# Performance work log

Hardware: AMD Instinct MI355X
Metric: run time of the kernel (lower is better)

Reference implementation:

```python
import jax, jax.numpy as jnp
import numpy as np

B, F, N = 8, 64, 256
EPS = 1e-09


def setup_inputs() -> dict:
    key = jax.random.key(0)
    k = jax.random.split(key, 4)
    x = jax.random.normal(k[0], (B, F, N, N), dtype=jnp.float32)
    mask = jax.random.randint(k[1], (B, N), 0, 2).astype(jnp.float32)
    weight = jnp.ones((1, F, 1, 1), dtype=jnp.float32)
    weight_exp = jax.random.normal(k[2], (1, F, 1, 1), dtype=jnp.float32)
    weight_bias = jnp.zeros((1, F, 1, 1), dtype=jnp.float32)
    bias = jax.random.normal(k[3], (1, F, 1), dtype=jnp.float32)
    return dict(x=x, mask=mask, weight=weight, weight_exp=weight_exp,
                weight_bias=weight_bias, bias=bias)


def reference(x, mask, weight, weight_exp, weight_bias, bias):
    # mask: [B, N] -> pairwise mask [B, 1, N, N] (broadcast over features,
    # same math as torch .expand to [B, F, N, N])
    m2 = mask[:, None, :, None] * mask[:, None, None, :]
    mdiag = mask * mask                       # diagonal of pairwise mask, [B, N]
    n = jnp.sum(mdiag, axis=-1, keepdims=True)  # [B, 1] (identical across F)
    n2 = jnp.clip(n - 1.0, 1.0)

    # trace(A * mask) per (b, f)
    diagA = jnp.einsum('bfii->bfi', x)
    trace = jnp.sum(diagA * mdiag[:, None, :], axis=-1)        # [B, F]
    # trace(A^2 * mask): diag(A @ A)_i = sum_k A[i,k] A[k,i]  (O(N^2), same math
    # as torch.linalg.matrix_power(A, 2) followed by masked diagonal trace)
    diagA2 = jnp.einsum('bfik,bfki->bfi', x, x)
    trace_sq = jnp.sum(diagA2 * mdiag[:, None, :], axis=-1)    # [B, F]

    mean = trace / n
    variance = trace_sq / n2 - trace ** 2 / (n * n2)
    mean_b = mean.mean(axis=1)      # [B]
    var_b = variance.mean(axis=1)   # [B]

    eye = jnp.eye(N, dtype=x.dtype)
    m_t = mean_b[:, None, None, None] * eye          # diag_embed of mean
    x_centered = (x - m_t) * m2
    x_norm = x_centered / jnp.sqrt(var_b[:, None, None, None] + EPS)

    bias_diag = bias[..., None] * eye                # [1, F, N, N] diag_embed
    return x_norm * (weight * jnp.exp(weight_exp) + weight_bias) + bias_diag
```

## Files before the change

kernel.cpp:

```cpp
#include <hip/hip_runtime.h>
#include <math.h>

#define BB 8
#define FF 64
#define NN 256
#define EPSF 1e-9f

typedef float floatx4 __attribute__((ext_vector_type(4)));


__global__ __launch_bounds__(256) void k_traces(const float* __restrict__ x,
                                                const float* __restrict__ mask,
                                                float* __restrict__ ws) {
    __shared__ float md[NN];
    __shared__ float T1[64][65];
    __shared__ float T2[64][65];
    __shared__ float red[4][2];
    const int t    = threadIdx.x;
    const int bh   = blockIdx.x;
    const int bf   = bh >> 1;
    const int half = bh & 1;
    const int b    = bf >> 6;
    const float* __restrict__ xm = x + (size_t)bf * (NN * NN);

    {
        float m = mask[b * NN + t];
        md[t] = m * m;
    }
    __syncthreads();

    const int lane = t & 63;
    const int w    = t >> 6;
    float acc2 = 0.f;
    float trp  = 0.f;

    constexpr int IT0[5] = {0, 1, 0, 0, 0};
    constexpr int KT0[5] = {0, 1, 1, 2, 3};
    constexpr int IT1[5] = {2, 3, 1, 1, 2};
    constexpr int KT1[5] = {2, 3, 2, 3, 3};

    #pragma unroll
    for (int e = 0; e < 5; ++e) {
        const int it = half ? IT1[e] : IT0[e];
        const int kt = half ? KT1[e] : KT0[e];
        const int i0 = it << 6;
        const int k0 = kt << 6;
        const bool diag = (it == kt);
        #pragma unroll
        for (int rr = 0; rr < 4; ++rr) {
            int idx4 = t + (rr << 8);
            int a    = idx4 >> 4;
            int c4   = (idx4 & 15) << 2;
            float4 v = *(const float4*)(xm + (size_t)(i0 + a) * NN + k0 + c4);
            T1[a][c4 + 0] = v.x; T1[a][c4 + 1] = v.y;
            T1[a][c4 + 2] = v.z; T1[a][c4 + 3] = v.w;
            if (!diag) {
                float4 u = *(const float4*)(xm + (size_t)(k0 + a) * NN + i0 + c4);
                T2[a][c4 + 0] = u.x; T2[a][c4 + 1] = u.y;
                T2[a][c4 + 2] = u.z; T2[a][c4 + 3] = u.w;
            }
        }
        __syncthreads();
        if (!diag) {
            #pragma unroll
            for (int s = 0; s < 16; ++s) {
                int a = w + (s << 2);
                acc2 += T1[a][lane] * T2[lane][a] * (md[i0 + a] + md[k0 + lane]);
            }
        } else {
            #pragma unroll
            for (int s = 0; s < 16; ++s) {
                int a = w + (s << 2);
                acc2 += T1[a][lane] * T1[lane][a] * md[i0 + a];
                if (lane == a) trp += T1[a][a] * md[i0 + a];
            }
        }
        __syncthreads();
    }

    #pragma unroll
    for (int off = 32; off > 0; off >>= 1) {
        acc2 += __shfl_down(acc2, off);
        trp  += __shfl_down(trp,  off);
    }
    if (lane == 0) { red[w][0] = trp; red[w][1] = acc2; }
    __syncthreads();
    if (t == 0) {
        float trace = red[0][0] + red[1][0] + red[2][0] + red[3][0];
        float tsq   = red[0][1] + red[1][1] + red[2][1] + red[3][1];
        ws[bh]        = trace;
        ws[1024 + bh] = tsq;
    }
}

__global__ __launch_bounds__(512) void k_finish(const float* __restrict__ mask,
                                                const float* __restrict__ wt,
                                                const float* __restrict__ wexp,
                                                const float* __restrict__ wbias,
                                                float* __restrict__ ws) {
    const int t    = threadIdx.x;
    const int b    = t >> 6;
    const int lane = t & 63;
    float trace = ws[2 * t] + ws[2 * t + 1];
    float tsq   = ws[1024 + 2 * t] + ws[1024 + 2 * t + 1];
    float tr2   = trace * trace;
    float nn = 0.f;
    #pragma unroll
    for (int r = 0; r < 4; ++r) {
        float m = mask[b * NN + lane + (r << 6)];
        nn += m * m;
    }
    #pragma unroll
    for (int off = 32; off > 0; off >>= 1) {
        trace += __shfl_down(trace, off);
        tr2   += __shfl_down(tr2, off);
        tsq   += __shfl_down(tsq, off);
        nn    += __shfl_down(nn, off);
    }
    if (lane == 0) {
        float n  = nn;
        float n2 = fmaxf(n - 1.f, 1.f);
        float mean_b = trace / (64.f * n);
        float var_b  = tsq / (64.f * n2) - tr2 / (64.f * n * n2);
        ws[2048 + b] = mean_b;
        ws[2056 + b] = 1.f / sqrtf(var_b + EPSF);
    }
    if (t < FF) ws[2064 + t] = wt[t] * expf(wexp[t]) + wbias[t];
}

__global__ __launch_bounds__(256) void k_out(const float* __restrict__ x,
                                             const float* __restrict__ mask,
                                             const float* __restrict__ bias,
                                             const float* __restrict__ ws,
                                             float* __restrict__ out) {
    const int total4 = (BB * FF * NN * NN) >> 2;
    const int stride = gridDim.x * blockDim.x;
    for (int idx4 = blockIdx.x * blockDim.x + threadIdx.x; idx4 < total4; idx4 += stride) {
        int e = idx4 << 2;
        int j = e & (NN - 1);
        int i = (e >> 8) & (NN - 1);
        int f = (e >> 16) & (FF - 1);
        int b = e >> 22;
        float4 xv = ((const float4*)x)[idx4];
        float  mi = mask[(b << 8) + i];
        float4 mj = ((const float4*)mask)[((b << 8) + j) >> 2];
        float meanb   = ws[2048 + b];
        float inv_std = ws[2056 + b];
        float g  = ws[2064 + f];
        float bs = bias[f];
        float s  = mi * inv_std * g;
        floatx4 o;
        o.x = (xv.x - (i == j     ? meanb : 0.f)) * mj.x * s + (i == j     ? bs : 0.f);
        o.y = (xv.y - (i == j + 1 ? meanb : 0.f)) * mj.y * s + (i == j + 1 ? bs : 0.f);
        o.z = (xv.z - (i == j + 2 ? meanb : 0.f)) * mj.z * s + (i == j + 2 ? bs : 0.f);
        o.w = (xv.w - (i == j + 3 ? meanb : 0.f)) * mj.w * s + (i == j + 3 ? bs : 0.f);
        __builtin_nontemporal_store(o, &((floatx4*)out)[idx4]);
    }
}

extern "C" void kernel_launch(void* const* d_in, const int* in_sizes, int n_in,
                              void* d_out, int out_size, void* d_ws, size_t ws_size,
                              hipStream_t stream) {
    const float* x     = (const float*)d_in[0];
    const float* mask  = (const float*)d_in[1];
    const float* wt    = (const float*)d_in[2];
    const float* wexp  = (const float*)d_in[3];
    const float* wbias = (const float*)d_in[4];
    const float* bias  = (const float*)d_in[5];
    float* out = (float*)d_out;
    float* ws  = (float*)d_ws;

    hipLaunchKernelGGL(k_traces, dim3(BB * FF * 2), dim3(256), 0, stream, x, mask, ws);
    hipLaunchKernelGGL(k_finish, dim3(1),           dim3(512), 0, stream, mask, wt, wexp, wbias, ws);
    hipLaunchKernelGGL(k_out,    dim3(2048),        dim3(256), 0, stream, x, mask, bias, ws, out);
}
```

Baseline: 66.41 us.

## Fold finish kernel into output kernel and register-prefetch trace tiles

Removes the single-block finish kernel: every block of the output kernel now recomputes per-batch mean, inverse std and the per-feature gains from the partial traces and keeps them in shared memory. This drops one launch and its serialized tail, at the cost of 2048 blocks each repeating the small reduction. The trace kernel also prefetches the next tile pair into registers while the current tile is being computed, so global loads overlap the LDS compute. Tile ordering is fixed so that the first two steps are the diagonal tiles.

```diff
diff --git a/kernel.cpp b/kernel.cpp
--- a/kernel.cpp
+++ b/kernel.cpp
@@ -8,6 +8,17 @@
 
 typedef float floatx4 __attribute__((ext_vector_type(4)));
 
+
+__device__ __forceinline__ int jit(int half, int e) {
+    constexpr int IT0[5] = {0, 1, 0, 0, 0};
+    constexpr int IT1[5] = {2, 3, 1, 1, 2};
+    return half ? IT1[e] : IT0[e];
+}
+__device__ __forceinline__ int jkt(int half, int e) {
+    constexpr int KT0[5] = {0, 1, 1, 2, 3};
+    constexpr int KT1[5] = {2, 3, 2, 3, 3};
+    return half ? KT1[e] : KT0[e];
+}
 
 __global__ __launch_bounds__(256) void k_traces(const float* __restrict__ x,
                                                 const float* __restrict__ mask,
@@ -23,44 +34,55 @@
     const int b    = bf >> 6;
     const float* __restrict__ xm = x + (size_t)bf * (NN * NN);
 
-    {
-        float m = mask[b * NN + t];
-        md[t] = m * m;
-    }
-    __syncthreads();
+    { float m = mask[b * NN + t]; md[t] = m * m; }
 
     const int lane = t & 63;
     const int w    = t >> 6;
-    float acc2 = 0.f;
-    float trp  = 0.f;
+    const int la   = t >> 4;
+    const int lc4  = (t & 15) << 2;
+    float acc2 = 0.f, trp = 0.f;
 
-    constexpr int IT0[5] = {0, 1, 0, 0, 0};
-    constexpr int KT0[5] = {0, 1, 1, 2, 3};
-    constexpr int IT1[5] = {2, 3, 1, 1, 2};
-    constexpr int KT1[5] = {2, 3, 2, 3, 3};
+    float4 p1[4], p2[4];
+
+    {
+        const int i0 = jit(half, 0) << 6, k0 = jkt(half, 0) << 6;
+        #pragma unroll
+        for (int rr = 0; rr < 4; ++rr) {
+            int a = la + (rr << 4);
+            p1[rr] = *(const float4*)(xm + (size_t)(i0 + a) * NN + k0 + lc4);
+        }
+    }
 
     #pragma unroll
     for (int e = 0; e < 5; ++e) {
-        const int it = half ? IT1[e] : IT0[e];
-        const int kt = half ? KT1[e] : KT0[e];
-        const int i0 = it << 6;
-        const int k0 = kt << 6;
-        const bool diag = (it == kt);
+        const bool diag = (e < 2);
+        const int i0 = jit(half, e) << 6;
+        const int k0 = jkt(half, e) << 6;
+
         #pragma unroll
         for (int rr = 0; rr < 4; ++rr) {
-            int idx4 = t + (rr << 8);
-            int a    = idx4 >> 4;
-            int c4   = (idx4 & 15) << 2;
-            float4 v = *(const float4*)(xm + (size_t)(i0 + a) * NN + k0 + c4);
-            T1[a][c4 + 0] = v.x; T1[a][c4 + 1] = v.y;
-            T1[a][c4 + 2] = v.z; T1[a][c4 + 3] = v.w;
+            int a = la + (rr << 4);
+            T1[a][lc4 + 0] = p1[rr].x; T1[a][lc4 + 1] = p1[rr].y;
+            T1[a][lc4 + 2] = p1[rr].z; T1[a][lc4 + 3] = p1[rr].w;
             if (!diag) {
-                float4 u = *(const float4*)(xm + (size_t)(k0 + a) * NN + i0 + c4);
-                T2[a][c4 + 0] = u.x; T2[a][c4 + 1] = u.y;
-                T2[a][c4 + 2] = u.z; T2[a][c4 + 3] = u.w;
+                T2[a][lc4 + 0] = p2[rr].x; T2[a][lc4 + 1] = p2[rr].y;
+                T2[a][lc4 + 2] = p2[rr].z; T2[a][lc4 + 3] = p2[rr].w;
             }
         }
         __syncthreads();
+
+        if (e < 4) {
+            const int ni0 = jit(half, e + 1) << 6;
+            const int nk0 = jkt(half, e + 1) << 6;
+            #pragma unroll
+            for (int rr = 0; rr < 4; ++rr) {
+                int a = la + (rr << 4);
+                p1[rr] = *(const float4*)(xm + (size_t)(ni0 + a) * NN + nk0 + lc4);
+                if (e + 1 >= 2)
+                    p2[rr] = *(const float4*)(xm + (size_t)(nk0 + a) * NN + ni0 + lc4);
+            }
+        }
+
         if (!diag) {
             #pragma unroll
             for (int s = 0; s < 16; ++s) {
@@ -86,56 +108,54 @@
     if (lane == 0) { red[w][0] = trp; red[w][1] = acc2; }
     __syncthreads();
     if (t == 0) {
-        float trace = red[0][0] + red[1][0] + red[2][0] + red[3][0];
-        float tsq   = red[0][1] + red[1][1] + red[2][1] + red[3][1];
-        ws[bh]        = trace;
-        ws[1024 + bh] = tsq;
+        ws[bh]        = red[0][0] + red[1][0] + red[2][0] + red[3][0];
+        ws[1024 + bh] = red[0][1] + red[1][1] + red[2][1] + red[3][1];
     }
-}
-
-__global__ __launch_bounds__(512) void k_finish(const float* __restrict__ mask,
-                                                const float* __restrict__ wt,
-                                                const float* __restrict__ wexp,
-                                                const float* __restrict__ wbias,
-                                                float* __restrict__ ws) {
-    const int t    = threadIdx.x;
-    const int b    = t >> 6;
-    const int lane = t & 63;
-    float trace = ws[2 * t] + ws[2 * t + 1];
-    float tsq   = ws[1024 + 2 * t] + ws[1024 + 2 * t + 1];
-    float tr2   = trace * trace;
-    float nn = 0.f;
-    #pragma unroll
-    for (int r = 0; r < 4; ++r) {
-        float m = mask[b * NN + lane + (r << 6)];
-        nn += m * m;
-    }
-    #pragma unroll
-    for (int off = 32; off > 0; off >>= 1) {
-        trace += __shfl_down(trace, off);
-        tr2   += __shfl_down(tr2, off);
-        tsq   += __shfl_down(tsq, off);
-        nn    += __shfl_down(nn, off);
-    }
-    if (lane == 0) {
-        float n  = nn;
-        float n2 = fmaxf(n - 1.f, 1.f);
-        float mean_b = trace / (64.f * n);
-        float var_b  = tsq / (64.f * n2) - tr2 / (64.f * n * n2);
-        ws[2048 + b] = mean_b;
-        ws[2056 + b] = 1.f / sqrtf(var_b + EPSF);
-    }
-    if (t < FF) ws[2064 + t] = wt[t] * expf(wexp[t]) + wbias[t];
 }
 
 __global__ __launch_bounds__(256) void k_out(const float* __restrict__ x,
                                              const float* __restrict__ mask,
+                                             const float* __restrict__ wt,
+                                             const float* __restrict__ wexp,
+                                             const float* __restrict__ wbias,
                                              const float* __restrict__ bias,
                                              const float* __restrict__ ws,
                                              float* __restrict__ out) {
+    __shared__ float smean[BB], sistd[BB], sg[FF], sb[FF];
+    const int t    = threadIdx.x;
+    const int lane = t & 63;
+    const int w    = t >> 6;
+
+    for (int bb = w; bb < BB; bb += 4) {
+        const int base = (bb << 7) + (lane << 1);
+        float trf = ws[base] + ws[base + 1];
+        float tsf = ws[1024 + base] + ws[1024 + base + 1];
+        float tr2 = trf * trf;
+        float m0 = mask[(bb << 8) + lane];
+        float m1 = mask[(bb << 8) + lane + 64];
+        float m2 = mask[(bb << 8) + lane + 128];
+        float m3 = mask[(bb << 8) + lane + 192];
+        float nn = m0 * m0 + m1 * m1 + m2 * m2 + m3 * m3;
+        #pragma unroll
+        for (int off = 32; off > 0; off >>= 1) {
+            trf += __shfl_down(trf, off);
+            tr2 += __shfl_down(tr2, off);
+            tsf += __shfl_down(tsf, off);
+            nn  += __shfl_down(nn,  off);
+        }
+        if (lane == 0) {
+            float n  = nn;
+            float n2 = fmaxf(n - 1.f, 1.f);
+            smean[bb] = trf / (64.f * n);
+            sistd[bb] = 1.f / sqrtf(tsf / (64.f * n2) - tr2 / (64.f * n * n2) + EPSF);
+        }
+    }
+    if (t < FF) { sg[t] = wt[t] * expf(wexp[t]) + wbias[t]; sb[t] = bias[t]; }
+    __syncthreads();
+
     const int total4 = (BB * FF * NN * NN) >> 2;
     const int stride = gridDim.x * blockDim.x;
-    for (int idx4 = blockIdx.x * blockDim.x + threadIdx.x; idx4 < total4; idx4 += stride) {
+    for (int idx4 = blockIdx.x * blockDim.x + t; idx4 < total4; idx4 += stride) {
         int e = idx4 << 2;
         int j = e & (NN - 1);
         int i = (e >> 8) & (NN - 1);
@@ -144,10 +164,10 @@
         float4 xv = ((const float4*)x)[idx4];
         float  mi = mask[(b << 8) + i];
         float4 mj = ((const float4*)mask)[((b << 8) + j) >> 2];
-        float meanb   = ws[2048 + b];
-        float inv_std = ws[2056 + b];
-        float g  = ws[2064 + f];
-        float bs = bias[f];
+        float meanb   = smean[b];
+        float inv_std = sistd[b];
+        float g  = sg[f];
+        float bs = sb[f];
         float s  = mi * inv_std * g;
         floatx4 o;
         o.x = (xv.x - (i == j     ? meanb : 0.f)) * mj.x * s + (i == j     ? bs : 0.f);
@@ -171,6 +191,6 @@
     float* ws  = (float*)d_ws;
 
     hipLaunchKernelGGL(k_traces, dim3(BB * FF * 2), dim3(256), 0, stream, x, mask, ws);
-    hipLaunchKernelGGL(k_finish, dim3(1),           dim3(512), 0, stream, mask, wt, wexp, wbias, ws);
-    hipLaunchKernelGGL(k_out,    dim3(2048),        dim3(256), 0, stream, x, mask, bias, ws, out);
+    hipLaunchKernelGGL(k_out,    dim3(2048),        dim3(256), 0, stream,
+                       x, mask, wt, wexp, wbias, bias, ws, out);
 }
```

Result: no change. 65.73 us (-1.0%).
